# Kernel tuning notes

Hardware: AMD Instinct MI355X
Metric: run time of the kernel (lower is better)

The kernel has to match this reference:

```python
import jax, jax.numpy as jnp
import numpy as np

NUM_LAYER = 5
EMB = 256
N = 100000
E = 300000
SELF_LOOP_BOND = 4
BN_EPS = 1e-5


def setup_inputs() -> dict:
    key = jax.random.key(0)
    ks = jax.random.split(key, 16)
    f = lambda k, shape: jax.random.normal(k, shape, jnp.float32) * 0.02
    return {
        "x_atom": jax.random.randint(ks[0], (N,), 0, 120),
        "x_chir": jax.random.randint(ks[1], (N,), 0, 3),
        "edge_index": jax.random.randint(ks[2], (2, E), 0, N),
        "edge_bond": jax.random.randint(ks[3], (E,), 0, 4),
        "edge_dir": jax.random.randint(ks[4], (E,), 0, 3),
        "atom_emb": f(ks[5], (120, EMB)),
        "chir_emb": f(ks[6], (3, EMB)),
        "bond_embs": f(ks[7], (NUM_LAYER, 6, EMB)),
        "dir_embs": f(ks[8], (NUM_LAYER, 3, EMB)),
        "W1s": f(ks[9], (NUM_LAYER, 2 * EMB, EMB)),
        "b1s": f(ks[10], (NUM_LAYER, 2 * EMB)),
        "W2s": f(ks[11], (NUM_LAYER, EMB, 2 * EMB)),
        "b2s": f(ks[12], (NUM_LAYER, EMB)),
        "bn_w": jnp.ones((NUM_LAYER, EMB), jnp.float32),
        "bn_b": jnp.zeros((NUM_LAYER, EMB), jnp.float32),
    }


def reference(x_atom, x_chir, edge_index, edge_bond, edge_dir,
              atom_emb, chir_emb, bond_embs, dir_embs,
              W1s, b1s, W2s, b2s, bn_w, bn_b):
    n = x_atom.shape[0]
    src, dst = edge_index[0], edge_index[1]
    # add self loops (edge_attr = [4, 0] for each node)
    loop = jnp.arange(n)
    src_full = jnp.concatenate([src, loop])          # [E+N]
    dst_full = jnp.concatenate([dst, loop])          # [E+N]
    bond_full = jnp.concatenate([edge_bond, jnp.full((n,), SELF_LOOP_BOND, edge_bond.dtype)])
    dir_full = jnp.concatenate([edge_dir, jnp.zeros((n,), edge_dir.dtype)])

    # initial node features: atom + chirality embeddings
    h = atom_emb[x_atom] + chir_emb[x_chir]          # [N, EMB]

    for l in range(NUM_LAYER):
        # per-layer edge embeddings (bond type + bond direction)
        e_emb = bond_embs[l][bond_full] + dir_embs[l][dir_full]   # [E+N, EMB]
        # message = x_j + edge_attr; aggregate = scatter-add to dst
        msg = h[src_full] + e_emb                                  # gather
        agg = jax.ops.segment_sum(msg, dst_full, num_segments=n)  # scatter-add
        # update MLP: Linear(EMB->2EMB) -> ReLU -> Linear(2EMB->EMB)
        hmid = jax.nn.relu(agg @ W1s[l].T + b1s[l])                # [N, 2EMB]
        h2 = hmid @ W2s[l].T + b2s[l]                              # [N, EMB]
        # batch norm (training mode: batch statistics, biased variance)
        mean = h2.mean(axis=0)
        var = h2.var(axis=0)
        h2 = (h2 - mean) * jax.lax.rsqrt(var + BN_EPS) * bn_w[l] + bn_b[l]
        # relu on all but last layer; dropout with p=0 is identity
        if l < NUM_LAYER - 1:
            h2 = jax.nn.relu(h2)
        h = h2
    # JK == 'last'
    return h
```

## Files before the change

kernel.cpp:

```cpp
#include <hip/hip_runtime.h>

#define EMB 256
#define NLAYER 5
#define CHUNK 1024

typedef unsigned int u32;
typedef unsigned short u16;

typedef __bf16 bf16x8 __attribute__((ext_vector_type(8)));
typedef float f32x4 __attribute__((ext_vector_type(4)));

__device__ __forceinline__ float bf2f(u16 u) {
    union { u32 i; float f; } x; x.i = ((u32)u) << 16; return x.f;
}
__device__ __forceinline__ u16 f2bf(float f) {
    union { float f; u32 i; } x; x.f = f;
    u32 r = x.i + 0x7FFFu + ((x.i >> 16) & 1u);
    return (u16)(r >> 16);
}
__device__ __forceinline__ u32 cvt_pk_bf16(float lo, float hi) {
    u32 r;
    asm("v_cvt_pk_bf16_f32 %0, %1, %2" : "=v"(r) : "v"(lo), "v"(hi));
    return r;
}
__device__ __forceinline__ void unpack4(uint2 p, float* o) {
    union { u32 i; float f; } a, b, c, d;
    a.i = p.x << 16; b.i = p.x & 0xFFFF0000u;
    c.i = p.y << 16; d.i = p.y & 0xFFFF0000u;
    o[0] = a.f; o[1] = b.f; o[2] = c.f; o[3] = d.f;
}

__global__ void k_detect(const u32* __restrict__ bnw_raw, int* __restrict__ flag) {
    if (threadIdx.x == 0 && blockIdx.x == 0)
        *flag = (bnw_raw[0] == 0x3F803F80u) ? 1 : 0;
}

struct Cvt { const void* s; u16* d; int n; };
struct CvtTab { Cvt t[10]; };

__global__ void k_convert(CvtTab tab, const int* __restrict__ flag, int maxn) {
    int f = *flag;
    int stride = gridDim.x * blockDim.x;
    for (int i = blockIdx.x * blockDim.x + threadIdx.x; i < maxn; i += stride) {
        for (int j = 0; j < 10; j++) {
            if (i < tab.t[j].n) {
                u16 v;
                if (f) v = ((const u16*)tab.t[j].s)[i];
                else   v = f2bf(((const float*)tab.t[j].s)[i]);
                tab.t[j].d[i] = v;
            }
        }
    }
}

__global__ void k_zero(u32* p, int n) {
    int i = blockIdx.x * blockDim.x + threadIdx.x;
    if (i < n) p[i] = 0u;
}

__global__ void k_hist(const int* __restrict__ eidx, const int* __restrict__ ebond,
                       const int* __restrict__ edir,
                       u32* __restrict__ cnt, u32* __restrict__ cntb, u32* __restrict__ cntd, int E) {
    int e = blockIdx.x * blockDim.x + threadIdx.x;
    if (e >= E) return;
    int dst = eidx[E + e];
    atomicAdd(&cnt[dst], 1u);
    atomicAdd(&cntb[dst * 4 + ebond[e]], 1u);
    atomicAdd(&cntd[dst * 3 + edir[e]], 1u);
}

__global__ void k_chunksum(const u32* __restrict__ cnt, u32* __restrict__ partial, int N) {
    int b = blockIdx.x, t = threadIdx.x;
    int base = b * CHUNK + t * 4;
    u32 s = 0;
    for (int i = 0; i < 4; i++) { int idx = base + i; if (idx < N) s += cnt[idx]; }
    __shared__ u32 red[256];
    red[t] = s; __syncthreads();
    for (int o = 128; o > 0; o >>= 1) { if (t < o) red[t] += red[t + o]; __syncthreads(); }
    if (t == 0) partial[b] = red[0];
}

__global__ void k_scanpartial(u32* partial, u32* indptr, int nch, int N) {
    if (threadIdx.x == 0 && blockIdx.x == 0) {
        u32 run = 0;
        for (int i = 0; i < nch; i++) { u32 x = partial[i]; partial[i] = run; run += x; }
        indptr[N] = run;
    }
}

__global__ void k_chunkscan(const u32* __restrict__ cnt, const u32* __restrict__ partial,
                            u32* __restrict__ indptr, u32* __restrict__ fillp, int N) {
    int b = blockIdx.x, t = threadIdx.x;
    int base = b * CHUNK + t * 4;
    u32 c[4]; u32 tsum = 0;
    for (int i = 0; i < 4; i++) { int idx = base + i; c[i] = (idx < N) ? cnt[idx] : 0u; tsum += c[i]; }
    __shared__ u32 sc[256];
    sc[t] = tsum; __syncthreads();
    for (int o = 1; o < 256; o <<= 1) {
        u32 x = (t >= o) ? sc[t - o] : 0u;
        __syncthreads();
        sc[t] += x;
        __syncthreads();
    }
    u32 run = partial[b] + sc[t] - tsum;
    for (int i = 0; i < 4; i++) {
        int idx = base + i;
        if (idx < N) { indptr[idx] = run; fillp[idx] = run; }
        run += c[i];
    }
}

__global__ void k_fill(const int* __restrict__ eidx, u32* __restrict__ fillp,
                       u32* __restrict__ srcs, int E) {
    int e = blockIdx.x * blockDim.x + threadIdx.x;
    if (e >= E) return;
    int dst = eidx[E + e];
    u32 pos = atomicAdd(&fillp[dst], 1u);
    srcs[pos] = (u32)eidx[e];
}

__global__ void k_h0(const int* __restrict__ xa, const int* __restrict__ xc,
                     const u16* __restrict__ aemb, const u16* __restrict__ cemb,
                     u16* __restrict__ H, int N) {
    int wave = threadIdx.x >> 6, lane = threadIdx.x & 63;
    int v = blockIdx.x * 4 + wave;
    if (v >= N) return;
    int a = xa[v], c = xc[v];
    int c4 = lane * 4;
    uint2 pa = *(const uint2*)(aemb + (size_t)a * EMB + c4);
    uint2 pc = *(const uint2*)(cemb + (size_t)c * EMB + c4);
    float fa[4], fc[4];
    unpack4(pa, fa); unpack4(pc, fc);
    ushort4 ov;
    ov.x = f2bf(fa[0] + fc[0]); ov.y = f2bf(fa[1] + fc[1]);
    ov.z = f2bf(fa[2] + fc[2]); ov.w = f2bf(fa[3] + fc[3]);
    *(ushort4*)(H + (size_t)v * EMB + c4) = ov;
}

__global__ void k_scatter(const u16* __restrict__ H, const u32* __restrict__ indptr,
                          const u32* __restrict__ srcs,
                          const u32* __restrict__ cntb, const u32* __restrict__ cntd,
                          const u16* __restrict__ bemb, const u16* __restrict__ demb,
                          const float* __restrict__ scsh, int relu,
                          u16* __restrict__ AGG, int N) {
    int wave = threadIdx.x >> 6, lane = threadIdx.x & 63;
    int v = blockIdx.x * 4 + wave;
    if (v >= N) return;
    int c4 = lane * 4;
    float sc[4] = {1.f, 1.f, 1.f, 1.f}, sh[4] = {0.f, 0.f, 0.f, 0.f};
    if (scsh) {
        float4 s0 = *(const float4*)(scsh + c4);
        float4 s1 = *(const float4*)(scsh + 256 + c4);
        sc[0] = s0.x; sc[1] = s0.y; sc[2] = s0.z; sc[3] = s0.w;
        sh[0] = s1.x; sh[1] = s1.y; sh[2] = s1.z; sh[3] = s1.w;
    }
    float acc[4] = {0.f, 0.f, 0.f, 0.f};
    u32 beg = indptr[v], end = indptr[v + 1];
    for (u32 e = beg; e < end; e++) {
        u32 s = srcs[e];
        uint2 p = *(const uint2*)(H + (size_t)s * EMB + c4);
        float f[4]; unpack4(p, f);
        for (int i = 0; i < 4; i++) {
            float y = f[i] * sc[i] + sh[i];
            if (relu) y = fmaxf(y, 0.f);
            acc[i] += y;
        }
    }
    {
        uint2 p = *(const uint2*)(H + (size_t)v * EMB + c4);
        float f[4]; unpack4(p, f);
        for (int i = 0; i < 4; i++) {
            float y = f[i] * sc[i] + sh[i];
            if (relu) y = fmaxf(y, 0.f);
            acc[i] += y;
        }
    }
    float cb[5];
    cb[0] = (float)cntb[v * 4 + 0]; cb[1] = (float)cntb[v * 4 + 1];
    cb[2] = (float)cntb[v * 4 + 2]; cb[3] = (float)cntb[v * 4 + 3]; cb[4] = 1.f;
    float cd[3];
    cd[0] = (float)cntd[v * 3 + 0] + 1.f; cd[1] = (float)cntd[v * 3 + 1]; cd[2] = (float)cntd[v * 3 + 2];
    for (int b = 0; b < 5; b++) {
        uint2 p = *(const uint2*)(bemb + b * EMB + c4);
        float f[4]; unpack4(p, f);
        for (int i = 0; i < 4; i++) acc[i] += cb[b] * f[i];
    }
    for (int d = 0; d < 3; d++) {
        uint2 p = *(const uint2*)(demb + d * EMB + c4);
        float f[4]; unpack4(p, f);
        for (int i = 0; i < 4; i++) acc[i] += cd[d] * f[i];
    }
    ushort4 ov;
    ov.x = f2bf(acc[0]); ov.y = f2bf(acc[1]); ov.z = f2bf(acc[2]); ov.w = f2bf(acc[3]);
    *(ushort4*)(AGG + (size_t)v * EMB + c4) = ov;
}

#define KP 264
#define HSS 272

__global__ __launch_bounds__(256, 2) void k_fused(
    const u16* __restrict__ A, const u16* __restrict__ W1, const u16* __restrict__ b1,
    const u16* __restrict__ W2, const u16* __restrict__ b2,
    u16* __restrict__ C, float* __restrict__ S, int M) {
    __shared__ __align__(16) u16 As[64 * KP];
    __shared__ __align__(16) u16 Hs[64 * HSS];
    int m0 = blockIdx.x * 64;
    int t = threadIdx.x;
    int wave = t >> 6, lane = t & 63;
    int lr = lane & 15, quad = lane >> 4;
    int wq = wave * 64;
    int wn = wave * 64;

    for (int it = 0; it < 8; it++) {
        int ci = t + it * 256;
        int r = ci >> 5, kc = (ci & 31) * 8;
        int gr = m0 + r; if (gr > M - 1) gr = M - 1;
        *(uint4*)(As + r * KP + kc) = *(const uint4*)(A + (size_t)gr * 256 + kc);
    }

    f32x4 acc2[4][4];
    #pragma unroll
    for (int i = 0; i < 4; i++)
        #pragma unroll
        for (int j = 0; j < 4; j++)
            acc2[i][j] = (f32x4){0.f, 0.f, 0.f, 0.f};

    __syncthreads();

    #pragma unroll
    for (int nh = 0; nh < 2; nh++) {
        f32x4 acc1[4][4];
        #pragma unroll
        for (int i = 0; i < 4; i++)
            #pragma unroll
            for (int j = 0; j < 4; j++)
                acc1[i][j] = (f32x4){0.f, 0.f, 0.f, 0.f};
        const u16* W1h = W1 + (size_t)(nh * 256) * 256;
        #pragma unroll
        for (int ks = 0; ks < 256; ks += 32) {
            bf16x8 af[4], wf[4];
            #pragma unroll
            for (int i = 0; i < 4; i++)
                af[i] = *(const bf16x8*)(As + (i * 16 + lr) * KP + ks + quad * 8);
            #pragma unroll
            for (int j = 0; j < 4; j++)
                wf[j] = *(const bf16x8*)(W1h + (size_t)(wq + j * 16 + lr) * 256 + ks + quad * 8);
            #pragma unroll
            for (int j = 0; j < 4; j++)
                #pragma unroll
                for (int i = 0; i < 4; i++)
                    acc1[i][j] = __builtin_amdgcn_mfma_f32_16x16x32_bf16(wf[j], af[i], acc1[i][j], 0, 0, 0);
        }
        __syncthreads();
        #pragma unroll
        for (int j = 0; j < 4; j++) {
            int wl = wq + j * 16 + quad * 4;
            ushort4 bq = *(const ushort4*)(b1 + nh * 256 + wl);
            float bv0 = bf2f(bq.x), bv1 = bf2f(bq.y), bv2 = bf2f(bq.z), bv3 = bf2f(bq.w);
            #pragma unroll
            for (int i = 0; i < 4; i++) {
                float v0 = fmaxf(acc1[i][j][0] + bv0, 0.f);
                float v1 = fmaxf(acc1[i][j][1] + bv1, 0.f);
                float v2 = fmaxf(acc1[i][j][2] + bv2, 0.f);
                float v3 = fmaxf(acc1[i][j][3] + bv3, 0.f);
                uint2 ov;
                ov.x = cvt_pk_bf16(v0, v1);
                ov.y = cvt_pk_bf16(v2, v3);
                *(uint2*)(Hs + (i * 16 + lr) * HSS + wl) = ov;
            }
        }
        __syncthreads();
        const u16* W2h = W2 + nh * 256;
        #pragma unroll
        for (int ks = 0; ks < 256; ks += 32) {
            bf16x8 hf[4], vf[4];
            #pragma unroll
            for (int i = 0; i < 4; i++)
                hf[i] = *(const bf16x8*)(Hs + (i * 16 + lr) * HSS + ks + quad * 8);
            #pragma unroll
            for (int j = 0; j < 4; j++)
                vf[j] = *(const bf16x8*)(W2h + (size_t)(wn + j * 16 + lr) * 512 + ks + quad * 8);
            #pragma unroll
            for (int i = 0; i < 4; i++)
                #pragma unroll
                for (int j = 0; j < 4; j++)
                    acc2[i][j] = __builtin_amdgcn_mfma_f32_16x16x32_bf16(hf[i], vf[j], acc2[i][j], 0, 0, 0);
        }
    }

    #pragma unroll
    for (int j = 0; j < 4; j++) {
        int gn = wn + j * 16 + lr;
        float bv = bf2f(b2[gn]);
        float s = 0.f, q = 0.f;
        #pragma unroll
        for (int i = 0; i < 4; i++) {
            int mbase = m0 + i * 16 + quad * 4;
            #pragma unroll
            for (int r = 0; r < 4; r++) {
                int gm = mbase + r;
                if (gm < M) {
                    float v = acc2[i][j][r] + bv;
                    C[(size_t)gm * 256 + gn] = f2bf(v);
                    s += v; q += v * v;
                }
            }
        }
        s += __shfl_xor(s, 16, 64); s += __shfl_xor(s, 32, 64);
        q += __shfl_xor(q, 16, 64); q += __shfl_xor(q, 32, 64);
        if (quad == 0) {
            atomicAdd(&S[gn], s);
            atomicAdd(&S[256 + gn], q);
        }
    }
}

__global__ void k_finalize(const float* __restrict__ S, const u16* __restrict__ bnw,
                           const u16* __restrict__ bnb, float* __restrict__ scsh, float invN) {
    int c = threadIdx.x;
    float mean = S[c] * invN;
    float var = S[256 + c] * invN - mean * mean;
    var = fmaxf(var, 0.f);
    float inv = rsqrtf(var + 1e-5f);
    float sc = bf2f(bnw[c]) * inv;
    scsh[c] = sc;
    scsh[256 + c] = bf2f(bnb[c]) - mean * sc;
}

__global__ void k_out(const u16* __restrict__ H2, const float* __restrict__ scsh,
                      void* __restrict__ out, const int* __restrict__ flag, int N) {
    int wave = threadIdx.x >> 6, lane = threadIdx.x & 63;
    int v = blockIdx.x * 4 + wave;
    if (v >= N) return;
    int c4 = lane * 4;
    float4 s0 = *(const float4*)(scsh + c4);
    float4 s1 = *(const float4*)(scsh + 256 + c4);
    uint2 p = *(const uint2*)(H2 + (size_t)v * EMB + c4);
    float f[4]; unpack4(p, f);
    float o0 = f[0] * s0.x + s1.x;
    float o1 = f[1] * s0.y + s1.y;
    float o2 = f[2] * s0.z + s1.z;
    float o3 = f[3] * s0.w + s1.w;
    if (*flag) {
        ushort4 ov;
        ov.x = f2bf(o0); ov.y = f2bf(o1); ov.z = f2bf(o2); ov.w = f2bf(o3);
        *(ushort4*)((u16*)out + (size_t)v * EMB + c4) = ov;
    } else {
        float4 ov = make_float4(o0, o1, o2, o3);
        *(float4*)((float*)out + (size_t)v * EMB + c4) = ov;
    }
}

extern "C" void kernel_launch(void* const* d_in, const int* in_sizes, int n_in,
                              void* d_out, int out_size, void* d_ws, size_t ws_size,
                              hipStream_t stream) {
    const int* x_atom = (const int*)d_in[0];
    const int* x_chir = (const int*)d_in[1];
    const int* eidx   = (const int*)d_in[2];
    const int* ebond  = (const int*)d_in[3];
    const int* edir   = (const int*)d_in[4];

    const int N = in_sizes[0];
    const int E = in_sizes[3];

    char* p = (char*)d_ws;
    size_t off = 0;
    auto alloc = [&](size_t bytes) -> void* {
        void* r = p + off;
        off += bytes;
        off = (off + 255) & ~(size_t)255;
        return r;
    };
    u16* X   = (u16*)alloc((size_t)N * EMB * 2);
    u16* Y   = (u16*)alloc((size_t)N * EMB * 2);
    u32* cz  = (u32*)alloc(((size_t)8 * N + NLAYER * 512) * 4);
    u32* cnt  = cz;
    u32* cntb = cz + N;
    u32* cntd = cz + 5 * (size_t)N;
    float* stats5 = (float*)(cz + 8 * (size_t)N);
    u32* indptr = (u32*)alloc((size_t)(N + 1) * 4);
    u32* fillp  = (u32*)alloc((size_t)N * 4);
    u32* srcs   = (u32*)alloc((size_t)E * 4);
    u32* partial = (u32*)alloc(256 * 4);
    float* scsh  = (float*)alloc(512 * 4);
    int* flag    = (int*)alloc(256);

    int csz[10] = {120 * EMB, 3 * EMB, NLAYER * 6 * EMB, NLAYER * 3 * EMB,
                   NLAYER * 512 * EMB, NLAYER * 512, NLAYER * EMB * 512, NLAYER * EMB,
                   NLAYER * EMB, NLAYER * EMB};
    u16* cbuf[10];
    for (int j = 0; j < 10; j++) cbuf[j] = (u16*)alloc((size_t)csz[j] * 2);
    u16* atom_emb  = cbuf[0];
    u16* chir_emb  = cbuf[1];
    u16* bond_embs = cbuf[2];
    u16* dir_embs  = cbuf[3];
    u16* W1s = cbuf[4];
    u16* b1s = cbuf[5];
    u16* W2s = cbuf[6];
    u16* b2s = cbuf[7];
    u16* bnw = cbuf[8];
    u16* bnb = cbuf[9];

    const int nodeBlocks = (N + 3) / 4;
    const int nch = (N + CHUNK - 1) / CHUNK;

    k_detect<<<1, 64, 0, stream>>>((const u32*)d_in[13], flag);
    {
        CvtTab tab;
        int maxn = 0;
        for (int j = 0; j < 10; j++) {
            tab.t[j].s = d_in[5 + j];
            tab.t[j].d = cbuf[j];
            tab.t[j].n = csz[j];
            if (csz[j] > maxn) maxn = csz[j];
        }
        k_convert<<<(maxn + 255) / 256, 256, 0, stream>>>(tab, flag, maxn);
    }

    {
        int z = 8 * N + NLAYER * 512;
        k_zero<<<(z + 255) / 256, 256, 0, stream>>>(cz, z);
    }
    k_hist<<<(E + 255) / 256, 256, 0, stream>>>(eidx, ebond, edir, cnt, cntb, cntd, E);
    k_chunksum<<<nch, 256, 0, stream>>>(cnt, partial, N);
    k_scanpartial<<<1, 64, 0, stream>>>(partial, indptr, nch, N);
    k_chunkscan<<<nch, 256, 0, stream>>>(cnt, partial, indptr, fillp, N);
    k_fill<<<(E + 255) / 256, 256, 0, stream>>>(eidx, fillp, srcs, E);

    k_h0<<<nodeBlocks, 256, 0, stream>>>(x_atom, x_chir, atom_emb, chir_emb, X, N);

    u16* H = X;
    u16* A = Y;
    const int mT64 = (N + 63) / 64;
    for (int l = 0; l < NLAYER; l++) {
        const u16* bemb = bond_embs + (size_t)l * 6 * EMB;
        const u16* demb = dir_embs + (size_t)l * 3 * EMB;
        const u16* W1 = W1s + (size_t)l * 512 * EMB;
        const u16* B1 = b1s + (size_t)l * 512;
        const u16* W2 = W2s + (size_t)l * EMB * 512;
        const u16* B2 = b2s + (size_t)l * EMB;
        float* stats = stats5 + (size_t)l * 512;

        k_scatter<<<nodeBlocks, 256, 0, stream>>>(H, indptr, srcs, cntb, cntd, bemb, demb,
                                                  (l == 0) ? nullptr : scsh, (l == 0) ? 0 : 1,
                                                  A, N);
        k_fused<<<mT64, 256, 0, stream>>>(A, W1, B1, W2, B2, A, stats, N);
        k_finalize<<<1, 256, 0, stream>>>(stats, bnw + (size_t)l * EMB, bnb + (size_t)l * EMB,
                                          scsh, 1.0f / (float)N);
        u16* tmp = H; H = A; A = tmp;
    }

    k_out<<<nodeBlocks, 256, 0, stream>>>(H, scsh, d_out, flag, N);
}
```

Baseline: 1.312 ms.

## Load A fragments directly from global and compute full hidden tile before second GEMM

The fused MLP kernel no longer stages the input tile in LDS. Each wave loads its A fragments directly from global memory (cache-served, since all waves read the same rows). The whole 64x512 ReLU hidden tile is now written to LDS before a single 512-deep second GEMM, which cuts the per-half __syncthreads to one barrier. The LDS footprint stays similar, but A is re-read from global/L2 for both halves and by every wave, so memory traffic and latency rise in exchange for fewer barriers.

```diff
diff --git a/kernel.cpp b/kernel.cpp
--- a/kernel.cpp
+++ b/kernel.cpp
@@ -195,37 +195,25 @@
     *(ushort4*)(AGG + (size_t)v * EMB + c4) = ov;
 }
 
-#define KP 264
-#define HSS 272
+#define HSF 528
 
 __global__ __launch_bounds__(256, 2) void k_fused(
     const u16* __restrict__ A, const u16* __restrict__ W1, const u16* __restrict__ b1,
     const u16* __restrict__ W2, const u16* __restrict__ b2,
     u16* __restrict__ C, float* __restrict__ S, int M) {
-    __shared__ __align__(16) u16 As[64 * KP];
-    __shared__ __align__(16) u16 Hs[64 * HSS];
+    __shared__ __align__(16) u16 Hs[64 * HSF];
     int m0 = blockIdx.x * 64;
     int t = threadIdx.x;
     int wave = t >> 6, lane = t & 63;
     int lr = lane & 15, quad = lane >> 4;
     int wq = wave * 64;
-    int wn = wave * 64;
-
-    for (int it = 0; it < 8; it++) {
-        int ci = t + it * 256;
-        int r = ci >> 5, kc = (ci & 31) * 8;
-        int gr = m0 + r; if (gr > M - 1) gr = M - 1;
-        *(uint4*)(As + r * KP + kc) = *(const uint4*)(A + (size_t)gr * 256 + kc);
-    }
-
-    f32x4 acc2[4][4];
+
+    const u16* ap[4];
     #pragma unroll
-    for (int i = 0; i < 4; i++)
-        #pragma unroll
-        for (int j = 0; j < 4; j++)
-            acc2[i][j] = (f32x4){0.f, 0.f, 0.f, 0.f};
-
-    __syncthreads();
+    for (int i = 0; i < 4; i++) {
+        int gr = m0 + i * 16 + lr; if (gr > M - 1) gr = M - 1;
+        ap[i] = A + (size_t)gr * 256 + quad * 8;
+    }
 
     #pragma unroll
     for (int nh = 0; nh < 2; nh++) {
@@ -235,27 +223,26 @@
             #pragma unroll
             for (int j = 0; j < 4; j++)
                 acc1[i][j] = (f32x4){0.f, 0.f, 0.f, 0.f};
-        const u16* W1h = W1 + (size_t)(nh * 256) * 256;
+        const u16* wp = W1 + (size_t)(nh * 256 + wq + lr) * 256 + quad * 8;
         #pragma unroll
         for (int ks = 0; ks < 256; ks += 32) {
             bf16x8 af[4], wf[4];
             #pragma unroll
+            for (int j = 0; j < 4; j++)
+                wf[j] = *(const bf16x8*)(wp + (size_t)j * 16 * 256 + ks);
+            #pragma unroll
             for (int i = 0; i < 4; i++)
-                af[i] = *(const bf16x8*)(As + (i * 16 + lr) * KP + ks + quad * 8);
-            #pragma unroll
-            for (int j = 0; j < 4; j++)
-                wf[j] = *(const bf16x8*)(W1h + (size_t)(wq + j * 16 + lr) * 256 + ks + quad * 8);
+                af[i] = *(const bf16x8*)(ap[i] + ks);
             #pragma unroll
             for (int j = 0; j < 4; j++)
                 #pragma unroll
                 for (int i = 0; i < 4; i++)
                     acc1[i][j] = __builtin_amdgcn_mfma_f32_16x16x32_bf16(wf[j], af[i], acc1[i][j], 0, 0, 0);
         }
-        __syncthreads();
         #pragma unroll
         for (int j = 0; j < 4; j++) {
-            int wl = wq + j * 16 + quad * 4;
-            ushort4 bq = *(const ushort4*)(b1 + nh * 256 + wl);
+            int wl = nh * 256 + wq + j * 16 + quad * 4;
+            ushort4 bq = *(const ushort4*)(b1 + wl);
             float bv0 = bf2f(bq.x), bv1 = bf2f(bq.y), bv2 = bf2f(bq.z), bv3 = bf2f(bq.w);
             #pragma unroll
             for (int i = 0; i < 4; i++) {
@@ -266,31 +253,38 @@
                 uint2 ov;
                 ov.x = cvt_pk_bf16(v0, v1);
                 ov.y = cvt_pk_bf16(v2, v3);
-                *(uint2*)(Hs + (i * 16 + lr) * HSS + wl) = ov;
+                *(uint2*)(Hs + (i * 16 + lr) * HSF + wl) = ov;
             }
         }
-        __syncthreads();
-        const u16* W2h = W2 + nh * 256;
-        #pragma unroll
-        for (int ks = 0; ks < 256; ks += 32) {
-            bf16x8 hf[4], vf[4];
-            #pragma unroll
-            for (int i = 0; i < 4; i++)
-                hf[i] = *(const bf16x8*)(Hs + (i * 16 + lr) * HSS + ks + quad * 8);
+    }
+    __syncthreads();
+
+    f32x4 acc2[4][4];
+    #pragma unroll
+    for (int i = 0; i < 4; i++)
+        #pragma unroll
+        for (int j = 0; j < 4; j++)
+            acc2[i][j] = (f32x4){0.f, 0.f, 0.f, 0.f};
+    const u16* vp = W2 + (size_t)(wq + lr) * 512 + quad * 8;
+    #pragma unroll
+    for (int ks = 0; ks < 512; ks += 32) {
+        bf16x8 hf[4], vf[4];
+        #pragma unroll
+        for (int j = 0; j < 4; j++)
+            vf[j] = *(const bf16x8*)(vp + (size_t)j * 16 * 512 + ks);
+        #pragma unroll
+        for (int i = 0; i < 4; i++)
+            hf[i] = *(const bf16x8*)(Hs + (i * 16 + lr) * HSF + ks + quad * 8);
+        #pragma unroll
+        for (int i = 0; i < 4; i++)
             #pragma unroll
             for (int j = 0; j < 4; j++)
-                vf[j] = *(const bf16x8*)(W2h + (size_t)(wn + j * 16 + lr) * 512 + ks + quad * 8);
-            #pragma unroll
-            for (int i = 0; i < 4; i++)
-                #pragma unroll
-                for (int j = 0; j < 4; j++)
-                    acc2[i][j] = __builtin_amdgcn_mfma_f32_16x16x32_bf16(hf[i], vf[j], acc2[i][j], 0, 0, 0);
-        }
+                acc2[i][j] = __builtin_amdgcn_mfma_f32_16x16x32_bf16(hf[i], vf[j], acc2[i][j], 0, 0, 0);
     }
 
     #pragma unroll
     for (int j = 0; j < 4; j++) {
-        int gn = wn + j * 16 + lr;
+        int gn = wq + j * 16 + lr;
         float bv = bf2f(b2[gn]);
         float s = 0.f, q = 0.f;
         #pragma unroll
```

Result: slower. 1.488 ms (+13.5%).
